# Optimization experiments

Measured on AMD Instinct MI355X. Metric: run time of the kernel, lower is better.

The kernel has to match this reference:

```python
import jax, jax.numpy as jnp
import numpy as np

R0 = 5.0
LEAK = 0.1
N_NODES = 50000
N_EDGES = 1600000
DIM_A = 32
DIM_V = 32


def setup_inputs() -> dict:
    key = jax.random.key(0)
    ks = jax.random.split(key, 10)
    s = 1.0 / np.sqrt(DIM_A)
    return {
        "r_ij": jax.random.normal(ks[0], (N_EDGES, 3), dtype=jnp.float32) * 2.0,
        "res_emb": jax.random.normal(ks[1], (N_NODES, DIM_A), dtype=jnp.float32),
        "src": jax.random.randint(ks[2], (N_EDGES,), 0, N_NODES, dtype=jnp.int64),
        "dst": jax.random.randint(ks[3], (N_EDGES,), 0, N_NODES, dtype=jnp.int64),
        "W1": jax.random.normal(ks[4], (DIM_A, DIM_A), dtype=jnp.float32) * s,
        "b1": jnp.zeros((DIM_A,), dtype=jnp.float32),
        "W2": jax.random.normal(ks[5], (DIM_A, DIM_A), dtype=jnp.float32) * s,
        "b2": jnp.zeros((DIM_A,), dtype=jnp.float32),
        "W3": jax.random.normal(ks[6], (DIM_A, DIM_A), dtype=jnp.float32) * s,
        "Wv": jax.random.normal(ks[7], (DIM_V, DIM_A), dtype=jnp.float32) * s,
    }


def _radial_encode(r, n, rmax):
    # r: [E, 3] -> [E, n]
    hn = (n + 1) // 2
    coeffs = (jnp.pi / rmax) * (1 + jnp.arange(hn) // 2).astype(r.dtype)
    dist = jnp.linalg.norm(r, axis=-1)[..., None]  # [E, 1]
    phase = coeffs * dist                           # [E, hn]
    return jnp.concatenate([jnp.cos(phase), jnp.sin(phase[..., : n - hn])], axis=-1)


def _leaky(x):
    return jnp.where(x >= 0, x, LEAK * x)


def _tens_sigmoid_vec(x):
    # Equivariant saturating nonlinearity on vectors: scale by tanh(|x|)/|x|.
    nrm = jnp.linalg.norm(x, axis=-1, keepdims=True)
    safe = jnp.where(nrm > 0, nrm, 1.0)
    return x * (jnp.tanh(nrm) / safe)


def reference(r_ij, res_emb, src, dst, W1, b1, W2, b2, W3, Wv):
    n_nodes = res_emb.shape[0]
    dim_a = W1.shape[1]
    # gather dst node features onto edges
    res_emb_j = res_emb[dst]                              # [E, dim_a]
    x = _radial_encode(r_ij, dim_a, R0) + res_emb_j       # [E, dim_a]
    h = _leaky(x @ W1.T + b1)
    h = _leaky(h @ W2.T + b2)
    rad_enc_ij = h @ W3.T                                 # [E, dim_a]
    rv = _tens_sigmoid_vec(r_ij * (7.0 / R0))             # [E, 3]
    phi_v = rad_enc_ij[..., None] * rv[:, None, :]        # [E, dim_a, 3]
    A_a = jax.ops.segment_sum(rad_enc_ij, src, num_segments=n_nodes)  # [N, dim_a]
    A_v = jax.ops.segment_sum(phi_v, src, num_segments=n_nodes)       # [N, dim_a, 3]
    out_v = jnp.einsum("nad,va->nvd", A_v, Wv)            # [N, dim_v, 3]
    return A_a, out_v
```

## Files before the change

kernel.cpp:

```cpp
#include <hip/hip_runtime.h>
#include <math.h>


#define NN 50000
#define NE 1600000
#define DA 32
#define PI_R0 0.62831853071795864769f
#define SCAN_BLOCKS 196
#define RSTRIDE 34

typedef float v2f __attribute__((ext_vector_type(2)));
typedef short bf16x8 __attribute__((ext_vector_type(8)));
typedef float f32x16 __attribute__((ext_vector_type(16)));

union frag_u { unsigned u[4]; bf16x8 v; };

__device__ __forceinline__ void wsync() {
    asm volatile("s_waitcnt lgkmcnt(0)" ::: "memory");
}

__device__ __forceinline__ unsigned cvt_pk(float lo, float hi) {
    unsigned r;
    asm("v_cvt_pk_bf16_f32 %0, %1, %2" : "=v"(r) : "v"(lo), "v"(hi));
    return r;
}

__device__ __forceinline__ float leaky(float x) {
    return fmaxf(x, 0.0f) + 0.1f * fminf(x, 0.0f);
}

__device__ __forceinline__ unsigned bf_hi(float x) {
    return (__float_as_uint(x) + 0x8000u) >> 16;
}
__device__ __forceinline__ unsigned bf_pack2(float lo, float hi) {
    return bf_hi(lo) | ((__float_as_uint(hi) + 0x8000u) & 0xffff0000u);
}


__global__ __launch_bounds__(256) void k_hist(const int* __restrict__ src,
                                              int* __restrict__ counts,
                                              int* __restrict__ rank) {
    const int e = blockIdx.x * 256 + threadIdx.x;
    rank[e] = atomicAdd(&counts[src[e]], 1);
}

__global__ __launch_bounds__(256) void k_scanA(const int* __restrict__ counts,
                                               int* __restrict__ bsum) {
    __shared__ int red[256];
    const int t = threadIdx.x;
    const int idx = blockIdx.x * 256 + t;
    red[t] = (idx < NN) ? counts[idx] : 0;
    __syncthreads();
    #pragma unroll
    for (int off = 128; off > 0; off >>= 1) {
        if (t < off) red[t] += red[t + off];
        __syncthreads();
    }
    if (t == 0) bsum[blockIdx.x] = red[0];
}

__global__ __launch_bounds__(256) void k_scanB(const int* __restrict__ bsum,
                                               int* __restrict__ bbase) {
    __shared__ int s[256];
    const int t = threadIdx.x;
    const int v = (t < SCAN_BLOCKS) ? bsum[t] : 0;
    s[t] = v;
    __syncthreads();
    #pragma unroll
    for (int off = 1; off < 256; off <<= 1) {
        const int x = s[t] + ((t >= off) ? s[t - off] : 0);
        __syncthreads();
        s[t] = x;
        __syncthreads();
    }
    if (t < SCAN_BLOCKS) bbase[t] = s[t] - v;
}

__global__ __launch_bounds__(256) void k_scanC(const int* __restrict__ counts,
                                               const int* __restrict__ bbase,
                                               int* __restrict__ offsets) {
    __shared__ int s[256];
    const int t = threadIdx.x;
    const int idx = blockIdx.x * 256 + t;
    const int v = (idx < NN) ? counts[idx] : 0;
    s[t] = v;
    __syncthreads();
    #pragma unroll
    for (int off = 1; off < 256; off <<= 1) {
        const int x = s[t] + ((t >= off) ? s[t - off] : 0);
        __syncthreads();
        s[t] = x;
        __syncthreads();
    }
    const int excl = s[t] - v + bbase[blockIdx.x];
    if (idx < NN) offsets[idx] = excl;
    if (idx == NN - 1) offsets[NN] = excl + v;
}

__global__ __launch_bounds__(256) void k_prep(
    const float* __restrict__ r_ij,
    const int*   __restrict__ src,
    const int*   __restrict__ dst,
    const int*   __restrict__ offsets,
    const int*   __restrict__ rank,
    uint4* __restrict__ rec)
{
    const int e = blockIdx.x * 256 + threadIdx.x;
    const int s = src[e];
    const int slot = offsets[s] + rank[e];

    const float rx = r_ij[(size_t)e*3 + 0];
    const float ry = r_ij[(size_t)e*3 + 1];
    const float rz = r_ij[(size_t)e*3 + 2];
    const float dist = sqrtf(rx*rx + ry*ry + rz*rz);

    const float nq = 1.4f * dist;
    const float e2 = __expf(2.0f * nq);
    const float sc14 = (nq > 0.0f)
        ? 1.4f * (e2 - 1.0f) * __builtin_amdgcn_rcpf((e2 + 1.0f) * nq)
        : 0.0f;

    uint4 r;
    r.x = __float_as_uint(dist);
    r.y = bf_pack2(rx * sc14, ry * sc14);
    r.z = bf_hi(rz * sc14);
    r.w = (unsigned)s | ((unsigned)dst[e] << 16);
    rec[slot] = r;
}

__global__ __launch_bounds__(256) void k_embcvt(const float* __restrict__ emb,
                                                unsigned* __restrict__ emb16) {
    const int t = blockIdx.x * 256 + threadIdx.x;
    emb16[t] = bf_pack2(emb[2*t], emb[2*t + 1]);
}


__global__ __launch_bounds__(256, 2) void dt_window(
    const uint4*    __restrict__ rec,
    const unsigned* __restrict__ emb16,
    const float* __restrict__ W1, const float* __restrict__ b1,
    const float* __restrict__ W2, const float* __restrict__ b2,
    const float* __restrict__ W3,
    float* __restrict__ A_a,
    float* __restrict__ out_v)
{
    __shared__ float  xrad[4][64][RSTRIDE];
    __shared__ float4 rvn_lds[4][64];

    const int tid  = threadIdx.x;
    const int wv   = tid >> 6;
    const int lane = tid & 63;
    const int g    = lane >> 5;
    const int m    = lane & 31;
    const int slot = blockIdx.x * 256 + tid;

    frag_u wf1[2], wf2[2], wf3[2];
    #pragma unroll
    for (int kt = 0; kt < 2; ++kt) {
        const float4 a1 = *(const float4*)&W1[m*DA + 16*kt + 4*g];
        const float4 c1 = *(const float4*)&W1[m*DA + 16*kt + 8 + 4*g];
        wf1[kt].u[0] = cvt_pk(a1.x, a1.y); wf1[kt].u[1] = cvt_pk(a1.z, a1.w);
        wf1[kt].u[2] = cvt_pk(c1.x, c1.y); wf1[kt].u[3] = cvt_pk(c1.z, c1.w);
        const float4 a2 = *(const float4*)&W2[m*DA + 16*kt + 4*g];
        const float4 c2 = *(const float4*)&W2[m*DA + 16*kt + 8 + 4*g];
        wf2[kt].u[0] = cvt_pk(a2.x, a2.y); wf2[kt].u[1] = cvt_pk(a2.z, a2.w);
        wf2[kt].u[2] = cvt_pk(c2.x, c2.y); wf2[kt].u[3] = cvt_pk(c2.z, c2.w);
        const float4 a3 = *(const float4*)&W3[m*DA + 16*kt + 4*g];
        const float4 c3 = *(const float4*)&W3[m*DA + 16*kt + 8 + 4*g];
        wf3[kt].u[0] = cvt_pk(a3.x, a3.y); wf3[kt].u[1] = cvt_pk(a3.z, a3.w);
        wf3[kt].u[2] = cvt_pk(c3.x, c3.y); wf3[kt].u[3] = cvt_pk(c3.z, c3.w);
    }

    const float4 b1q0 = *(const float4*)&b1[4*g];
    const float4 b1q1 = *(const float4*)&b1[8 + 4*g];
    const float4 b1q2 = *(const float4*)&b1[16 + 4*g];
    const float4 b1q3 = *(const float4*)&b1[24 + 4*g];
    const float4 b2q0 = *(const float4*)&b2[4*g];
    const float4 b2q1 = *(const float4*)&b2[8 + 4*g];
    const float4 b2q2 = *(const float4*)&b2[16 + 4*g];
    const float4 b2q3 = *(const float4*)&b2[24 + 4*g];

    const uint4 rc = rec[slot];
    const float dist = __uint_as_float(rc.x);
    const float vx = __uint_as_float(rc.y << 16);
    const float vy = __uint_as_float(rc.y & 0xffff0000u);
    const float vz = __uint_as_float(rc.z << 16);
    const int  node = (int)(rc.w & 0xffffu);
    const int  dn   = (int)(rc.w >> 16);

    v2f xa[16];
    #pragma unroll
    for (int mm = 0; mm < 8; ++mm) {
        float sph, cph;
        __sincosf(PI_R0 * (float)(mm + 1) * dist, &sph, &cph);
        xa[mm]     = (v2f){cph, cph};
        xa[8 + mm] = (v2f){sph, sph};
    }
    const uint4* ep = (const uint4*)(emb16 + (size_t)dn * 16);
    #pragma unroll
    for (int q = 0; q < 4; ++q) {
        const uint4 u = ep[q];
        xa[q*4 + 0] += (v2f){__uint_as_float(u.x << 16), __uint_as_float(u.x & 0xffff0000u)};
        xa[q*4 + 1] += (v2f){__uint_as_float(u.y << 16), __uint_as_float(u.y & 0xffff0000u)};
        xa[q*4 + 2] += (v2f){__uint_as_float(u.z << 16), __uint_as_float(u.z & 0xffff0000u)};
        xa[q*4 + 3] += (v2f){__uint_as_float(u.w << 16), __uint_as_float(u.w & 0xffff0000u)};
    }

    rvn_lds[wv][lane] = make_float4(vx, vy, vz, __int_as_float(node));

    {
        uint2* xr = (uint2*)&xrad[wv][lane][0];
        xr[0] = make_uint2(cvt_pk(xa[0].x,  xa[0].y),  cvt_pk(xa[1].x,  xa[1].y));
        xr[1] = make_uint2(cvt_pk(xa[2].x,  xa[2].y),  cvt_pk(xa[3].x,  xa[3].y));
        xr[2] = make_uint2(cvt_pk(xa[4].x,  xa[4].y),  cvt_pk(xa[5].x,  xa[5].y));
        xr[3] = make_uint2(cvt_pk(xa[6].x,  xa[6].y),  cvt_pk(xa[7].x,  xa[7].y));
        xr[4] = make_uint2(cvt_pk(xa[8].x,  xa[8].y),  cvt_pk(xa[9].x,  xa[9].y));
        xr[5] = make_uint2(cvt_pk(xa[10].x, xa[10].y), cvt_pk(xa[11].x, xa[11].y));
        xr[6] = make_uint2(cvt_pk(xa[12].x, xa[12].y), cvt_pk(xa[13].x, xa[13].y));
        xr[7] = make_uint2(cvt_pk(xa[14].x, xa[14].y), cvt_pk(xa[15].x, xa[15].y));
    }
    wsync();

    frag_u xf[2][2];
    #pragma unroll
    for (int t = 0; t < 2; ++t) {
        const unsigned* er = (const unsigned*)&xrad[wv][32*t + m][0];
        #pragma unroll
        for (int kt = 0; kt < 2; ++kt) {
            const uint2 qa = *(const uint2*)&er[8*kt + 2*g];
            const uint2 qb = *(const uint2*)&er[8*kt + 4 + 2*g];
            xf[t][kt].u[0] = qa.x; xf[t][kt].u[1] = qa.y;
            xf[t][kt].u[2] = qb.x; xf[t][kt].u[3] = qb.y;
        }
    }

    f32x16 acc0, acc1;
    acc0[0]=b1q0.x; acc0[1]=b1q0.y; acc0[2]=b1q0.z; acc0[3]=b1q0.w;
    acc0[4]=b1q1.x; acc0[5]=b1q1.y; acc0[6]=b1q1.z; acc0[7]=b1q1.w;
    acc0[8]=b1q2.x; acc0[9]=b1q2.y; acc0[10]=b1q2.z; acc0[11]=b1q2.w;
    acc0[12]=b1q3.x; acc0[13]=b1q3.y; acc0[14]=b1q3.z; acc0[15]=b1q3.w;
    acc1 = acc0;
    acc0 = __builtin_amdgcn_mfma_f32_32x32x16_bf16(wf1[0].v, xf[0][0].v, acc0, 0, 0, 0);
    acc0 = __builtin_amdgcn_mfma_f32_32x32x16_bf16(wf1[1].v, xf[0][1].v, acc0, 0, 0, 0);
    acc1 = __builtin_amdgcn_mfma_f32_32x32x16_bf16(wf1[0].v, xf[1][0].v, acc1, 0, 0, 0);
    acc1 = __builtin_amdgcn_mfma_f32_32x32x16_bf16(wf1[1].v, xf[1][1].v, acc1, 0, 0, 0);

    frag_u hf[2][2];
    #pragma unroll
    for (int t = 0; t < 2; ++t) {
        const f32x16 a = t ? acc1 : acc0;
        float h[16];
        #pragma unroll
        for (int r = 0; r < 16; ++r) h[r] = leaky(a[r]);
        hf[t][0].u[0] = cvt_pk(h[0], h[1]);   hf[t][0].u[1] = cvt_pk(h[2], h[3]);
        hf[t][0].u[2] = cvt_pk(h[4], h[5]);   hf[t][0].u[3] = cvt_pk(h[6], h[7]);
        hf[t][1].u[0] = cvt_pk(h[8], h[9]);   hf[t][1].u[1] = cvt_pk(h[10], h[11]);
        hf[t][1].u[2] = cvt_pk(h[12], h[13]); hf[t][1].u[3] = cvt_pk(h[14], h[15]);
    }

    f32x16 c0, c1;
    c0[0]=b2q0.x; c0[1]=b2q0.y; c0[2]=b2q0.z; c0[3]=b2q0.w;
    c0[4]=b2q1.x; c0[5]=b2q1.y; c0[6]=b2q1.z; c0[7]=b2q1.w;
    c0[8]=b2q2.x; c0[9]=b2q2.y; c0[10]=b2q2.z; c0[11]=b2q2.w;
    c0[12]=b2q3.x; c0[13]=b2q3.y; c0[14]=b2q3.z; c0[15]=b2q3.w;
    c1 = c0;
    c0 = __builtin_amdgcn_mfma_f32_32x32x16_bf16(wf2[0].v, hf[0][0].v, c0, 0, 0, 0);
    c0 = __builtin_amdgcn_mfma_f32_32x32x16_bf16(wf2[1].v, hf[0][1].v, c0, 0, 0, 0);
    c1 = __builtin_amdgcn_mfma_f32_32x32x16_bf16(wf2[0].v, hf[1][0].v, c1, 0, 0, 0);
    c1 = __builtin_amdgcn_mfma_f32_32x32x16_bf16(wf2[1].v, hf[1][1].v, c1, 0, 0, 0);

    frag_u gf[2][2];
    #pragma unroll
    for (int t = 0; t < 2; ++t) {
        const f32x16 a = t ? c1 : c0;
        float h[16];
        #pragma unroll
        for (int r = 0; r < 16; ++r) h[r] = leaky(a[r]);
        gf[t][0].u[0] = cvt_pk(h[0], h[1]);   gf[t][0].u[1] = cvt_pk(h[2], h[3]);
        gf[t][0].u[2] = cvt_pk(h[4], h[5]);   gf[t][0].u[3] = cvt_pk(h[6], h[7]);
        gf[t][1].u[0] = cvt_pk(h[8], h[9]);   gf[t][1].u[1] = cvt_pk(h[10], h[11]);
        gf[t][1].u[2] = cvt_pk(h[12], h[13]); gf[t][1].u[3] = cvt_pk(h[14], h[15]);
    }

    f32x16 r0 = {}, r1 = {};
    r0 = __builtin_amdgcn_mfma_f32_32x32x16_bf16(wf3[0].v, gf[0][0].v, r0, 0, 0, 0);
    r0 = __builtin_amdgcn_mfma_f32_32x32x16_bf16(wf3[1].v, gf[0][1].v, r0, 0, 0, 0);
    r1 = __builtin_amdgcn_mfma_f32_32x32x16_bf16(wf3[0].v, gf[1][0].v, r1, 0, 0, 0);
    r1 = __builtin_amdgcn_mfma_f32_32x32x16_bf16(wf3[1].v, gf[1][1].v, r1, 0, 0, 0);

    #pragma unroll
    for (int t = 0; t < 2; ++t) {
        const f32x16 a = t ? r1 : r0;
        float* rr = &xrad[wv][32*t + m][0];
        *(float2*)&rr[4*g]          = make_float2(a[0],  a[1]);
        *(float2*)&rr[4*g + 2]      = make_float2(a[2],  a[3]);
        *(float2*)&rr[8 + 4*g]      = make_float2(a[4],  a[5]);
        *(float2*)&rr[8 + 4*g + 2]  = make_float2(a[6],  a[7]);
        *(float2*)&rr[16 + 4*g]     = make_float2(a[8],  a[9]);
        *(float2*)&rr[16 + 4*g + 2] = make_float2(a[10], a[11]);
        *(float2*)&rr[24 + 4*g]     = make_float2(a[12], a[13]);
        *(float2*)&rr[24 + 4*g + 2] = make_float2(a[14], a[15]);
    }
    wsync();

    const int p = lane >> 5;
    const int i = lane & 31;
    const int base = p << 5;

    float accA = 0.0f, a0 = 0.0f, a1 = 0.0f, a2 = 0.0f;
    int cur = __float_as_int(rvn_lds[wv][base].w);

    #pragma unroll 4
    for (int l = 0; l < 32; ++l) {
        const float4 rvn = rvn_lds[wv][base + l];
        const int nd = __float_as_int(rvn.w);
        const float rd = xrad[wv][base + l][i];
        if (nd != cur) {
            atomicAdd(&A_a[cur*DA + i], accA);
            atomicAdd(&out_v[(cur*DA + i)*3 + 0], a0);
            atomicAdd(&out_v[(cur*DA + i)*3 + 1], a1);
            atomicAdd(&out_v[(cur*DA + i)*3 + 2], a2);
            accA = a0 = a1 = a2 = 0.0f;
            cur = nd;
        }
        accA += rd;
        a0 += rd * rvn.x;
        a1 += rd * rvn.y;
        a2 += rd * rvn.z;
    }
    atomicAdd(&A_a[cur*DA + i], accA);
    atomicAdd(&out_v[(cur*DA + i)*3 + 0], a0);
    atomicAdd(&out_v[(cur*DA + i)*3 + 1], a1);
    atomicAdd(&out_v[(cur*DA + i)*3 + 2], a2);
}


__global__ __launch_bounds__(256) void dt_node(
    const float* __restrict__ Wv,
    float* Av_out)
{
    __shared__ float sWv[DA*DA];
    for (int i = threadIdx.x; i < DA*DA; i += 256) sWv[i] = Wv[i];
    __syncthreads();

    const int t = blockIdx.x * 256 + threadIdx.x;
    const int n = t >> 5;
    const int v = t & 31;

    const float* av = Av_out + (size_t)n * (DA*3);
    float o0 = 0.0f, o1 = 0.0f, o2 = 0.0f;
    #pragma unroll
    for (int a = 0; a < DA; ++a) {
        const float w = sWv[v*DA + a];
        o0 += w * av[a*3 + 0];
        o1 += w * av[a*3 + 1];
        o2 += w * av[a*3 + 2];
    }
    __syncthreads();
    float* o = Av_out + (size_t)n * (DA*3) + v*3;
    o[0] = o0; o[1] = o1; o[2] = o2;
}


__global__ __launch_bounds__(256) void k_scan_legacy(const int* __restrict__ counts,
                                                     int* __restrict__ offsets) {
    __shared__ int part[256];
    const int CH = (NN + 255) / 256;
    const int t = threadIdx.x;
    const int base = t * CH;
    int s = 0;
    for (int k = 0; k < CH; ++k) { const int idx = base + k; if (idx < NN) s += counts[idx]; }
    part[t] = s;
    __syncthreads();
    if (t == 0) {
        int run = 0;
        for (int k = 0; k < 256; ++k) { const int v = part[k]; part[k] = run; run += v; }
    }
    __syncthreads();
    int run = part[t];
    for (int k = 0; k < CH; ++k) {
        const int idx = base + k;
        if (idx < NN) { offsets[idx] = run; run += counts[idx]; }
    }
    if (t == 255) offsets[NN] = run;
}

__global__ __launch_bounds__(256) void k_scatter_legacy(const int* __restrict__ src,
                                                        const int* __restrict__ offsets,
                                                        const int* __restrict__ rank,
                                                        int* __restrict__ edge_ids) {
    const int e = blockIdx.x * 256 + threadIdx.x;
    edge_ids[offsets[src[e]] + rank[e]] = e;
}

__global__ __launch_bounds__(256, 2) void dt_window_legacy(
    const float* __restrict__ r_ij,
    const float* __restrict__ res_emb,
    const int*   __restrict__ src,
    const int*   __restrict__ dst,
    const int*   __restrict__ edge_ids,
    const float* __restrict__ W1, const float* __restrict__ b1,
    const float* __restrict__ W2, const float* __restrict__ b2,
    const float* __restrict__ W3,
    float* __restrict__ A_a,
    float* __restrict__ out_v)
{
    __shared__ float  rad_lds[4][32][36];
    __shared__ float4 rvn_lds[4][64];

    const int tid  = threadIdx.x;
    const int wv   = tid >> 6;
    const int lane = tid & 63;
    const int slot = blockIdx.x * 256 + tid;

    const int eid  = edge_ids[slot];
    const int node = src[eid];

    const float rx = r_ij[(size_t)eid*3 + 0];
    const float ry = r_ij[(size_t)eid*3 + 1];
    const float rz = r_ij[(size_t)eid*3 + 2];
    const float dist = sqrtf(rx*rx + ry*ry + rz*rz);

    float xa[DA], xb[DA];
    #pragma unroll
    for (int mm = 0; mm < 8; ++mm) {
        float sph, cph;
        __sincosf(PI_R0 * (float)(mm + 1) * dist, &sph, &cph);
        xa[2*mm] = cph; xa[2*mm+1] = cph;
        xa[16+2*mm] = sph; xa[16+2*mm+1] = sph;
    }
    const float4* er = (const float4*)(res_emb + (size_t)dst[eid] * DA);
    #pragma unroll
    for (int q = 0; q < 8; ++q) {
        const float4 v = er[q];
        xa[q*4+0] += v.x; xa[q*4+1] += v.y; xa[q*4+2] += v.z; xa[q*4+3] += v.w;
    }
    #pragma unroll
    for (int i = 0; i < DA; ++i) {
        float acc = b1[i];
        #pragma unroll
        for (int j = 0; j < DA; ++j) acc += W1[i*DA + j] * xa[j];
        xb[i] = (acc >= 0.0f) ? acc : 0.1f * acc;
    }
    #pragma unroll
    for (int i = 0; i < DA; ++i) {
        float acc = b2[i];
        #pragma unroll
        for (int j = 0; j < DA; ++j) acc += W2[i*DA + j] * xb[j];
        xa[i] = (acc >= 0.0f) ? acc : 0.1f * acc;
    }
    #pragma unroll
    for (int i = 0; i < DA; ++i) {
        float acc = 0.0f;
        #pragma unroll
        for (int j = 0; j < DA; ++j) acc += W3[i*DA + j] * xa[j];
        xb[i] = acc;
    }

    const float qx = rx*1.4f, qy = ry*1.4f, qz = rz*1.4f;
    const float nq = sqrtf(qx*qx + qy*qy + qz*qz);
    const float e2 = __expf(2.0f * nq);
    const float sc = (nq > 0.0f)
        ? (e2 - 1.0f) * __builtin_amdgcn_rcpf((e2 + 1.0f) * nq)
        : 0.0f;

    rvn_lds[wv][lane] = make_float4(qx*sc, qy*sc, qz*sc, __int_as_float(node));

    const int p = lane >> 5;
    const int i = lane & 31;

    if (lane < 32) {
        float* rrow = rad_lds[wv][lane];
        #pragma unroll
        for (int q = 0; q < 8; ++q)
            *(float4*)&rrow[q*4] = make_float4(xb[q*4+0], xb[q*4+1], xb[q*4+2], xb[q*4+3]);
    }
    wsync();

    float accA = 0.0f, a0 = 0.0f, a1 = 0.0f, a2 = 0.0f;
    int cur = __float_as_int(rvn_lds[wv][0].w);

    #pragma unroll 4
    for (int l = 0; l < 32; ++l) {
        const float4 rvn = rvn_lds[wv][l];
        const int nd = __float_as_int(rvn.w);
        const float rd = rad_lds[wv][l][i];
        if (nd != cur) {
            if (p == 0) {
                atomicAdd(&A_a[cur*DA + i], accA);
                atomicAdd(&out_v[(cur*DA + i)*3 + 0], a0);
            } else {
                atomicAdd(&out_v[(cur*DA + i)*3 + 1], a1);
                atomicAdd(&out_v[(cur*DA + i)*3 + 2], a2);
            }
            accA = a0 = a1 = a2 = 0.0f;
            cur = nd;
        }
        accA += rd; a0 += rd*rvn.x; a1 += rd*rvn.y; a2 += rd*rvn.z;
    }
    wsync();
    if (lane >= 32) {
        float* rrow = rad_lds[wv][lane - 32];
        #pragma unroll
        for (int q = 0; q < 8; ++q)
            *(float4*)&rrow[q*4] = make_float4(xb[q*4+0], xb[q*4+1], xb[q*4+2], xb[q*4+3]);
    }
    wsync();
    #pragma unroll 4
    for (int l = 32; l < 64; ++l) {
        const float4 rvn = rvn_lds[wv][l];
        const int nd = __float_as_int(rvn.w);
        const float rd = rad_lds[wv][l - 32][i];
        if (nd != cur) {
            if (p == 0) {
                atomicAdd(&A_a[cur*DA + i], accA);
                atomicAdd(&out_v[(cur*DA + i)*3 + 0], a0);
            } else {
                atomicAdd(&out_v[(cur*DA + i)*3 + 1], a1);
                atomicAdd(&out_v[(cur*DA + i)*3 + 2], a2);
            }
            accA = a0 = a1 = a2 = 0.0f;
            cur = nd;
        }
        accA += rd; a0 += rd*rvn.x; a1 += rd*rvn.y; a2 += rd*rvn.z;
    }
    if (p == 0) {
        atomicAdd(&A_a[cur*DA + i], accA);
        atomicAdd(&out_v[(cur*DA + i)*3 + 0], a0);
    } else {
        atomicAdd(&out_v[(cur*DA + i)*3 + 1], a1);
        atomicAdd(&out_v[(cur*DA + i)*3 + 2], a2);
    }
}


extern "C" void kernel_launch(void* const* d_in, const int* in_sizes, int n_in,
                              void* d_out, int out_size, void* d_ws, size_t ws_size,
                              hipStream_t stream) {
    const float* r_ij    = (const float*)d_in[0];
    const float* res_emb = (const float*)d_in[1];
    const int*   src     = (const int*)d_in[2];
    const int*   dst     = (const int*)d_in[3];
    const float* W1      = (const float*)d_in[4];
    const float* b1      = (const float*)d_in[5];
    const float* W2      = (const float*)d_in[6];
    const float* b2      = (const float*)d_in[7];
    const float* W3      = (const float*)d_in[8];
    const float* Wv      = (const float*)d_in[9];

    float* A_a   = (float*)d_out;
    float* out_v = (float*)d_out + (size_t)NN * DA;

    const size_t need_new = ((size_t)NE*4 + (size_t)NN*16 + NN + NN + 1 + NE + 256 + 256) * sizeof(int);
    const size_t need_leg = ((size_t)NN + NN + 1 + NE + NE) * sizeof(int);

    hipMemsetAsync(d_out, 0, (size_t)out_size * sizeof(float), stream);

    if (ws_size >= need_new) {
        uint4*    rec     = (uint4*)d_ws;
        unsigned* emb16   = (unsigned*)(rec + NE);
        int*      counts  = (int*)(emb16 + (size_t)NN*16);
        int*      offsets = counts + NN;
        int*      rank    = offsets + NN + 1;
        int*      bsum    = rank + NE;
        int*      bbase   = bsum + 256;

        hipMemsetAsync(counts, 0, (size_t)NN * sizeof(int), stream);
        k_hist  <<<NE / 256, 256, 0, stream>>>(src, counts, rank);
        k_scanA <<<SCAN_BLOCKS, 256, 0, stream>>>(counts, bsum);
        k_scanB <<<1, 256, 0, stream>>>(bsum, bbase);
        k_scanC <<<SCAN_BLOCKS, 256, 0, stream>>>(counts, bbase, offsets);
        k_embcvt<<<(NN*16) / 256, 256, 0, stream>>>(res_emb, emb16);
        k_prep  <<<NE / 256, 256, 0, stream>>>(r_ij, src, dst, offsets, rank, rec);
        dt_window<<<NE / 256, 256, 0, stream>>>(rec, emb16,
                                                W1, b1, W2, b2, W3, A_a, out_v);
        dt_node <<<(NN * DA) / 256, 256, 0, stream>>>(Wv, out_v);
    } else if (ws_size >= need_leg) {
        int* counts   = (int*)d_ws;
        int* offsets  = counts + NN;
        int* rank     = offsets + NN + 1;
        int* edge_ids = rank + NE;

        hipMemsetAsync(counts, 0, (size_t)NN * sizeof(int), stream);
        k_hist          <<<NE / 256, 256, 0, stream>>>(src, counts, rank);
        k_scan_legacy   <<<1, 256, 0, stream>>>(counts, offsets);
        k_scatter_legacy<<<NE / 256, 256, 0, stream>>>(src, offsets, rank, edge_ids);
        dt_window_legacy<<<NE / 256, 256, 0, stream>>>(r_ij, res_emb, src, dst, edge_ids,
                                                       W1, b1, W2, b2, W3, A_a, out_v);
        dt_node         <<<(NN * DA) / 256, 256, 0, stream>>>(Wv, out_v);
    }
}
```

Baseline: 260.1 us.

## Split histogram bins per node, process 128 edges per wave, split atomics across half-waves

The counting-sort histogram now uses four sub-bins per source node, keyed by the low bits of the edge index. This spreads atomic contention on the counts array, and the scan is widened to handle the larger bin count. The edge MLP kernel now has each wave process two 64-edge batches and carries the segment accumulator across them, which halves the block count and cuts the flush atomics at batch boundaries. Each half-wave now issues only two of the four output atomics per flush instead of all four. Costs are a longer scan and sub-bins that interleave edges of the same node, though they stay contiguous per node.

```diff
diff --git a/kernel.cpp b/kernel.cpp
--- a/kernel.cpp
+++ b/kernel.cpp
@@ -5,8 +5,9 @@
 #define NN 50000
 #define NE 1600000
 #define DA 32
+#define NB (NN*4)
 #define PI_R0 0.62831853071795864769f
-#define SCAN_BLOCKS 196
+#define SCANB_BLOCKS 782
 #define RSTRIDE 34
 
 typedef float v2f __attribute__((ext_vector_type(2)));
@@ -41,7 +42,8 @@
                                               int* __restrict__ counts,
                                               int* __restrict__ rank) {
     const int e = blockIdx.x * 256 + threadIdx.x;
-    rank[e] = atomicAdd(&counts[src[e]], 1);
+    const int key = (src[e] << 2) | (e & 3);
+    rank[e] = atomicAdd(&counts[key], 1);
 }
 
 __global__ __launch_bounds__(256) void k_scanA(const int* __restrict__ counts,
@@ -49,7 +51,7 @@
     __shared__ int red[256];
     const int t = threadIdx.x;
     const int idx = blockIdx.x * 256 + t;
-    red[t] = (idx < NN) ? counts[idx] : 0;
+    red[t] = (idx < NB) ? counts[idx] : 0;
     __syncthreads();
     #pragma unroll
     for (int off = 128; off > 0; off >>= 1) {
@@ -59,21 +61,21 @@
     if (t == 0) bsum[blockIdx.x] = red[0];
 }
 
-__global__ __launch_bounds__(256) void k_scanB(const int* __restrict__ bsum,
-                                               int* __restrict__ bbase) {
-    __shared__ int s[256];
+__global__ __launch_bounds__(1024) void k_scanB(const int* __restrict__ bsum,
+                                                int* __restrict__ bbase) {
+    __shared__ int s[1024];
     const int t = threadIdx.x;
-    const int v = (t < SCAN_BLOCKS) ? bsum[t] : 0;
+    const int v = (t < SCANB_BLOCKS) ? bsum[t] : 0;
     s[t] = v;
     __syncthreads();
     #pragma unroll
-    for (int off = 1; off < 256; off <<= 1) {
+    for (int off = 1; off < 1024; off <<= 1) {
         const int x = s[t] + ((t >= off) ? s[t - off] : 0);
         __syncthreads();
         s[t] = x;
         __syncthreads();
     }
-    if (t < SCAN_BLOCKS) bbase[t] = s[t] - v;
+    if (t < SCANB_BLOCKS) bbase[t] = s[t] - v;
 }
 
 __global__ __launch_bounds__(256) void k_scanC(const int* __restrict__ counts,
@@ -82,7 +84,7 @@
     __shared__ int s[256];
     const int t = threadIdx.x;
     const int idx = blockIdx.x * 256 + t;
-    const int v = (idx < NN) ? counts[idx] : 0;
+    const int v = (idx < NB) ? counts[idx] : 0;
     s[t] = v;
     __syncthreads();
     #pragma unroll
@@ -93,8 +95,8 @@
         __syncthreads();
     }
     const int excl = s[t] - v + bbase[blockIdx.x];
-    if (idx < NN) offsets[idx] = excl;
-    if (idx == NN - 1) offsets[NN] = excl + v;
+    if (idx < NB) offsets[idx] = excl;
+    if (idx == NB - 1) offsets[NB] = excl + v;
 }
 
 __global__ __launch_bounds__(256) void k_prep(
@@ -107,7 +109,7 @@
 {
     const int e = blockIdx.x * 256 + threadIdx.x;
     const int s = src[e];
-    const int slot = offsets[s] + rank[e];
+    const int slot = offsets[(s << 2) | (e & 3)] + rank[e];
 
     const float rx = r_ij[(size_t)e*3 + 0];
     const float ry = r_ij[(size_t)e*3 + 1];
@@ -147,12 +149,12 @@
     __shared__ float  xrad[4][64][RSTRIDE];
     __shared__ float4 rvn_lds[4][64];
 
-    const int tid  = threadIdx.x;
-    const int wv   = tid >> 6;
-    const int lane = tid & 63;
-    const int g    = lane >> 5;
-    const int m    = lane & 31;
-    const int slot = blockIdx.x * 256 + tid;
+    const int tid   = threadIdx.x;
+    const int wv    = tid >> 6;
+    const int lane  = tid & 63;
+    const int g     = lane >> 5;
+    const int m     = lane & 31;
+    const int wbase = blockIdx.x * 512 + wv * 128;
 
     frag_u wf1[2], wf2[2], wf3[2];
     #pragma unroll
@@ -180,158 +182,171 @@
     const float4 b2q2 = *(const float4*)&b2[16 + 4*g];
     const float4 b2q3 = *(const float4*)&b2[24 + 4*g];
 
-    const uint4 rc = rec[slot];
-    const float dist = __uint_as_float(rc.x);
-    const float vx = __uint_as_float(rc.y << 16);
-    const float vy = __uint_as_float(rc.y & 0xffff0000u);
-    const float vz = __uint_as_float(rc.z << 16);
-    const int  node = (int)(rc.w & 0xffffu);
-    const int  dn   = (int)(rc.w >> 16);
-
-    v2f xa[16];
-    #pragma unroll
-    for (int mm = 0; mm < 8; ++mm) {
-        float sph, cph;
-        __sincosf(PI_R0 * (float)(mm + 1) * dist, &sph, &cph);
-        xa[mm]     = (v2f){cph, cph};
-        xa[8 + mm] = (v2f){sph, sph};
-    }
-    const uint4* ep = (const uint4*)(emb16 + (size_t)dn * 16);
-    #pragma unroll
-    for (int q = 0; q < 4; ++q) {
-        const uint4 u = ep[q];
-        xa[q*4 + 0] += (v2f){__uint_as_float(u.x << 16), __uint_as_float(u.x & 0xffff0000u)};
-        xa[q*4 + 1] += (v2f){__uint_as_float(u.y << 16), __uint_as_float(u.y & 0xffff0000u)};
-        xa[q*4 + 2] += (v2f){__uint_as_float(u.z << 16), __uint_as_float(u.z & 0xffff0000u)};
-        xa[q*4 + 3] += (v2f){__uint_as_float(u.w << 16), __uint_as_float(u.w & 0xffff0000u)};
-    }
-
-    rvn_lds[wv][lane] = make_float4(vx, vy, vz, __int_as_float(node));
-
-    {
-        uint2* xr = (uint2*)&xrad[wv][lane][0];
-        xr[0] = make_uint2(cvt_pk(xa[0].x,  xa[0].y),  cvt_pk(xa[1].x,  xa[1].y));
-        xr[1] = make_uint2(cvt_pk(xa[2].x,  xa[2].y),  cvt_pk(xa[3].x,  xa[3].y));
-        xr[2] = make_uint2(cvt_pk(xa[4].x,  xa[4].y),  cvt_pk(xa[5].x,  xa[5].y));
-        xr[3] = make_uint2(cvt_pk(xa[6].x,  xa[6].y),  cvt_pk(xa[7].x,  xa[7].y));
-        xr[4] = make_uint2(cvt_pk(xa[8].x,  xa[8].y),  cvt_pk(xa[9].x,  xa[9].y));
-        xr[5] = make_uint2(cvt_pk(xa[10].x, xa[10].y), cvt_pk(xa[11].x, xa[11].y));
-        xr[6] = make_uint2(cvt_pk(xa[12].x, xa[12].y), cvt_pk(xa[13].x, xa[13].y));
-        xr[7] = make_uint2(cvt_pk(xa[14].x, xa[14].y), cvt_pk(xa[15].x, xa[15].y));
-    }
-    wsync();
-
-    frag_u xf[2][2];
-    #pragma unroll
-    for (int t = 0; t < 2; ++t) {
-        const unsigned* er = (const unsigned*)&xrad[wv][32*t + m][0];
-        #pragma unroll
-        for (int kt = 0; kt < 2; ++kt) {
-            const uint2 qa = *(const uint2*)&er[8*kt + 2*g];
-            const uint2 qb = *(const uint2*)&er[8*kt + 4 + 2*g];
-            xf[t][kt].u[0] = qa.x; xf[t][kt].u[1] = qa.y;
-            xf[t][kt].u[2] = qb.x; xf[t][kt].u[3] = qb.y;
-        }
-    }
-
-    f32x16 acc0, acc1;
-    acc0[0]=b1q0.x; acc0[1]=b1q0.y; acc0[2]=b1q0.z; acc0[3]=b1q0.w;
-    acc0[4]=b1q1.x; acc0[5]=b1q1.y; acc0[6]=b1q1.z; acc0[7]=b1q1.w;
-    acc0[8]=b1q2.x; acc0[9]=b1q2.y; acc0[10]=b1q2.z; acc0[11]=b1q2.w;
-    acc0[12]=b1q3.x; acc0[13]=b1q3.y; acc0[14]=b1q3.z; acc0[15]=b1q3.w;
-    acc1 = acc0;
-    acc0 = __builtin_amdgcn_mfma_f32_32x32x16_bf16(wf1[0].v, xf[0][0].v, acc0, 0, 0, 0);
-    acc0 = __builtin_amdgcn_mfma_f32_32x32x16_bf16(wf1[1].v, xf[0][1].v, acc0, 0, 0, 0);
-    acc1 = __builtin_amdgcn_mfma_f32_32x32x16_bf16(wf1[0].v, xf[1][0].v, acc1, 0, 0, 0);
-    acc1 = __builtin_amdgcn_mfma_f32_32x32x16_bf16(wf1[1].v, xf[1][1].v, acc1, 0, 0, 0);
-
-    frag_u hf[2][2];
-    #pragma unroll
-    for (int t = 0; t < 2; ++t) {
-        const f32x16 a = t ? acc1 : acc0;
-        float h[16];
-        #pragma unroll
-        for (int r = 0; r < 16; ++r) h[r] = leaky(a[r]);
-        hf[t][0].u[0] = cvt_pk(h[0], h[1]);   hf[t][0].u[1] = cvt_pk(h[2], h[3]);
-        hf[t][0].u[2] = cvt_pk(h[4], h[5]);   hf[t][0].u[3] = cvt_pk(h[6], h[7]);
-        hf[t][1].u[0] = cvt_pk(h[8], h[9]);   hf[t][1].u[1] = cvt_pk(h[10], h[11]);
-        hf[t][1].u[2] = cvt_pk(h[12], h[13]); hf[t][1].u[3] = cvt_pk(h[14], h[15]);
-    }
-
-    f32x16 c0, c1;
-    c0[0]=b2q0.x; c0[1]=b2q0.y; c0[2]=b2q0.z; c0[3]=b2q0.w;
-    c0[4]=b2q1.x; c0[5]=b2q1.y; c0[6]=b2q1.z; c0[7]=b2q1.w;
-    c0[8]=b2q2.x; c0[9]=b2q2.y; c0[10]=b2q2.z; c0[11]=b2q2.w;
-    c0[12]=b2q3.x; c0[13]=b2q3.y; c0[14]=b2q3.z; c0[15]=b2q3.w;
-    c1 = c0;
-    c0 = __builtin_amdgcn_mfma_f32_32x32x16_bf16(wf2[0].v, hf[0][0].v, c0, 0, 0, 0);
-    c0 = __builtin_amdgcn_mfma_f32_32x32x16_bf16(wf2[1].v, hf[0][1].v, c0, 0, 0, 0);
-    c1 = __builtin_amdgcn_mfma_f32_32x32x16_bf16(wf2[0].v, hf[1][0].v, c1, 0, 0, 0);
-    c1 = __builtin_amdgcn_mfma_f32_32x32x16_bf16(wf2[1].v, hf[1][1].v, c1, 0, 0, 0);
-
-    frag_u gf[2][2];
-    #pragma unroll
-    for (int t = 0; t < 2; ++t) {
-        const f32x16 a = t ? c1 : c0;
-        float h[16];
-        #pragma unroll
-        for (int r = 0; r < 16; ++r) h[r] = leaky(a[r]);
-        gf[t][0].u[0] = cvt_pk(h[0], h[1]);   gf[t][0].u[1] = cvt_pk(h[2], h[3]);
-        gf[t][0].u[2] = cvt_pk(h[4], h[5]);   gf[t][0].u[3] = cvt_pk(h[6], h[7]);
-        gf[t][1].u[0] = cvt_pk(h[8], h[9]);   gf[t][1].u[1] = cvt_pk(h[10], h[11]);
-        gf[t][1].u[2] = cvt_pk(h[12], h[13]); gf[t][1].u[3] = cvt_pk(h[14], h[15]);
-    }
-
-    f32x16 r0 = {}, r1 = {};
-    r0 = __builtin_amdgcn_mfma_f32_32x32x16_bf16(wf3[0].v, gf[0][0].v, r0, 0, 0, 0);
-    r0 = __builtin_amdgcn_mfma_f32_32x32x16_bf16(wf3[1].v, gf[0][1].v, r0, 0, 0, 0);
-    r1 = __builtin_amdgcn_mfma_f32_32x32x16_bf16(wf3[0].v, gf[1][0].v, r1, 0, 0, 0);
-    r1 = __builtin_amdgcn_mfma_f32_32x32x16_bf16(wf3[1].v, gf[1][1].v, r1, 0, 0, 0);
-
-    #pragma unroll
-    for (int t = 0; t < 2; ++t) {
-        const f32x16 a = t ? r1 : r0;
-        float* rr = &xrad[wv][32*t + m][0];
-        *(float2*)&rr[4*g]          = make_float2(a[0],  a[1]);
-        *(float2*)&rr[4*g + 2]      = make_float2(a[2],  a[3]);
-        *(float2*)&rr[8 + 4*g]      = make_float2(a[4],  a[5]);
-        *(float2*)&rr[8 + 4*g + 2]  = make_float2(a[6],  a[7]);
-        *(float2*)&rr[16 + 4*g]     = make_float2(a[8],  a[9]);
-        *(float2*)&rr[16 + 4*g + 2] = make_float2(a[10], a[11]);
-        *(float2*)&rr[24 + 4*g]     = make_float2(a[12], a[13]);
-        *(float2*)&rr[24 + 4*g + 2] = make_float2(a[14], a[15]);
-    }
-    wsync();
-
-    const int p = lane >> 5;
-    const int i = lane & 31;
-    const int base = p << 5;
-
+    const int p = g;
+    const int i = m;
     float accA = 0.0f, a0 = 0.0f, a1 = 0.0f, a2 = 0.0f;
-    int cur = __float_as_int(rvn_lds[wv][base].w);
-
-    #pragma unroll 4
-    for (int l = 0; l < 32; ++l) {
-        const float4 rvn = rvn_lds[wv][base + l];
-        const int nd = __float_as_int(rvn.w);
-        const float rd = xrad[wv][base + l][i];
-        if (nd != cur) {
-            atomicAdd(&A_a[cur*DA + i], accA);
-            atomicAdd(&out_v[(cur*DA + i)*3 + 0], a0);
-            atomicAdd(&out_v[(cur*DA + i)*3 + 1], a1);
-            atomicAdd(&out_v[(cur*DA + i)*3 + 2], a2);
-            accA = a0 = a1 = a2 = 0.0f;
-            cur = nd;
-        }
-        accA += rd;
-        a0 += rd * rvn.x;
-        a1 += rd * rvn.y;
-        a2 += rd * rvn.z;
-    }
-    atomicAdd(&A_a[cur*DA + i], accA);
-    atomicAdd(&out_v[(cur*DA + i)*3 + 0], a0);
-    atomicAdd(&out_v[(cur*DA + i)*3 + 1], a1);
-    atomicAdd(&out_v[(cur*DA + i)*3 + 2], a2);
+    int cur = -1;
+
+    #pragma unroll
+    for (int b = 0; b < 2; ++b) {
+        const int slot = wbase + b*64 + lane;
+
+        const uint4 rc = rec[slot];
+        const float dist = __uint_as_float(rc.x);
+        const float vx = __uint_as_float(rc.y << 16);
+        const float vy = __uint_as_float(rc.y & 0xffff0000u);
+        const float vz = __uint_as_float(rc.z << 16);
+        const int  node = (int)(rc.w & 0xffffu);
+        const int  dn   = (int)(rc.w >> 16);
+
+        v2f xa[16];
+        #pragma unroll
+        for (int mm = 0; mm < 8; ++mm) {
+            float sph, cph;
+            __sincosf(PI_R0 * (float)(mm + 1) * dist, &sph, &cph);
+            xa[mm]     = (v2f){cph, cph};
+            xa[8 + mm] = (v2f){sph, sph};
+        }
+        const uint4* ep = (const uint4*)(emb16 + (size_t)dn * 16);
+        #pragma unroll
+        for (int q = 0; q < 4; ++q) {
+            const uint4 u = ep[q];
+            xa[q*4 + 0] += (v2f){__uint_as_float(u.x << 16), __uint_as_float(u.x & 0xffff0000u)};
+            xa[q*4 + 1] += (v2f){__uint_as_float(u.y << 16), __uint_as_float(u.y & 0xffff0000u)};
+            xa[q*4 + 2] += (v2f){__uint_as_float(u.z << 16), __uint_as_float(u.z & 0xffff0000u)};
+            xa[q*4 + 3] += (v2f){__uint_as_float(u.w << 16), __uint_as_float(u.w & 0xffff0000u)};
+        }
+
+        rvn_lds[wv][lane] = make_float4(vx, vy, vz, __int_as_float(node));
+
+        {
+            uint2* xr = (uint2*)&xrad[wv][lane][0];
+            xr[0] = make_uint2(cvt_pk(xa[0].x,  xa[0].y),  cvt_pk(xa[1].x,  xa[1].y));
+            xr[1] = make_uint2(cvt_pk(xa[2].x,  xa[2].y),  cvt_pk(xa[3].x,  xa[3].y));
+            xr[2] = make_uint2(cvt_pk(xa[4].x,  xa[4].y),  cvt_pk(xa[5].x,  xa[5].y));
+            xr[3] = make_uint2(cvt_pk(xa[6].x,  xa[6].y),  cvt_pk(xa[7].x,  xa[7].y));
+            xr[4] = make_uint2(cvt_pk(xa[8].x,  xa[8].y),  cvt_pk(xa[9].x,  xa[9].y));
+            xr[5] = make_uint2(cvt_pk(xa[10].x, xa[10].y), cvt_pk(xa[11].x, xa[11].y));
+            xr[6] = make_uint2(cvt_pk(xa[12].x, xa[12].y), cvt_pk(xa[13].x, xa[13].y));
+            xr[7] = make_uint2(cvt_pk(xa[14].x, xa[14].y), cvt_pk(xa[15].x, xa[15].y));
+        }
+        wsync();
+
+        frag_u xf[2][2];
+        #pragma unroll
+        for (int t = 0; t < 2; ++t) {
+            const unsigned* er = (const unsigned*)&xrad[wv][32*t + m][0];
+            #pragma unroll
+            for (int kt = 0; kt < 2; ++kt) {
+                const uint2 qa = *(const uint2*)&er[8*kt + 2*g];
+                const uint2 qb = *(const uint2*)&er[8*kt + 4 + 2*g];
+                xf[t][kt].u[0] = qa.x; xf[t][kt].u[1] = qa.y;
+                xf[t][kt].u[2] = qb.x; xf[t][kt].u[3] = qb.y;
+            }
+        }
+
+        f32x16 acc0, acc1;
+        acc0[0]=b1q0.x; acc0[1]=b1q0.y; acc0[2]=b1q0.z; acc0[3]=b1q0.w;
+        acc0[4]=b1q1.x; acc0[5]=b1q1.y; acc0[6]=b1q1.z; acc0[7]=b1q1.w;
+        acc0[8]=b1q2.x; acc0[9]=b1q2.y; acc0[10]=b1q2.z; acc0[11]=b1q2.w;
+        acc0[12]=b1q3.x; acc0[13]=b1q3.y; acc0[14]=b1q3.z; acc0[15]=b1q3.w;
+        acc1 = acc0;
+        acc0 = __builtin_amdgcn_mfma_f32_32x32x16_bf16(wf1[0].v, xf[0][0].v, acc0, 0, 0, 0);
+        acc0 = __builtin_amdgcn_mfma_f32_32x32x16_bf16(wf1[1].v, xf[0][1].v, acc0, 0, 0, 0);
+        acc1 = __builtin_amdgcn_mfma_f32_32x32x16_bf16(wf1[0].v, xf[1][0].v, acc1, 0, 0, 0);
+        acc1 = __builtin_amdgcn_mfma_f32_32x32x16_bf16(wf1[1].v, xf[1][1].v, acc1, 0, 0, 0);
+
+        frag_u hf[2][2];
+        #pragma unroll
+        for (int t = 0; t < 2; ++t) {
+            const f32x16 a = t ? acc1 : acc0;
+            float h[16];
+            #pragma unroll
+            for (int r = 0; r < 16; ++r) h[r] = leaky(a[r]);
+            hf[t][0].u[0] = cvt_pk(h[0], h[1]);   hf[t][0].u[1] = cvt_pk(h[2], h[3]);
+            hf[t][0].u[2] = cvt_pk(h[4], h[5]);   hf[t][0].u[3] = cvt_pk(h[6], h[7]);
+            hf[t][1].u[0] = cvt_pk(h[8], h[9]);   hf[t][1].u[1] = cvt_pk(h[10], h[11]);
+            hf[t][1].u[2] = cvt_pk(h[12], h[13]); hf[t][1].u[3] = cvt_pk(h[14], h[15]);
+        }
+
+        f32x16 c0, c1;
+        c0[0]=b2q0.x; c0[1]=b2q0.y; c0[2]=b2q0.z; c0[3]=b2q0.w;
+        c0[4]=b2q1.x; c0[5]=b2q1.y; c0[6]=b2q1.z; c0[7]=b2q1.w;
+        c0[8]=b2q2.x; c0[9]=b2q2.y; c0[10]=b2q2.z; c0[11]=b2q2.w;
+        c0[12]=b2q3.x; c0[13]=b2q3.y; c0[14]=b2q3.z; c0[15]=b2q3.w;
+        c1 = c0;
+        c0 = __builtin_amdgcn_mfma_f32_32x32x16_bf16(wf2[0].v, hf[0][0].v, c0, 0, 0, 0);
+        c0 = __builtin_amdgcn_mfma_f32_32x32x16_bf16(wf2[1].v, hf[0][1].v, c0, 0, 0, 0);
+        c1 = __builtin_amdgcn_mfma_f32_32x32x16_bf16(wf2[0].v, hf[1][0].v, c1, 0, 0, 0);
+        c1 = __builtin_amdgcn_mfma_f32_32x32x16_bf16(wf2[1].v, hf[1][1].v, c1, 0, 0, 0);
+
+        frag_u gf[2][2];
+        #pragma unroll
+        for (int t = 0; t < 2; ++t) {
+            const f32x16 a = t ? c1 : c0;
+            float h[16];
+            #pragma unroll
+            for (int r = 0; r < 16; ++r) h[r] = leaky(a[r]);
+            gf[t][0].u[0] = cvt_pk(h[0], h[1]);   gf[t][0].u[1] = cvt_pk(h[2], h[3]);
+            gf[t][0].u[2] = cvt_pk(h[4], h[5]);   gf[t][0].u[3] = cvt_pk(h[6], h[7]);
+            gf[t][1].u[0] = cvt_pk(h[8], h[9]);   gf[t][1].u[1] = cvt_pk(h[10], h[11]);
+            gf[t][1].u[2] = cvt_pk(h[12], h[13]); gf[t][1].u[3] = cvt_pk(h[14], h[15]);
+        }
+
+        f32x16 r0 = {}, r1 = {};
+        r0 = __builtin_amdgcn_mfma_f32_32x32x16_bf16(wf3[0].v, gf[0][0].v, r0, 0, 0, 0);
+        r0 = __builtin_amdgcn_mfma_f32_32x32x16_bf16(wf3[1].v, gf[0][1].v, r0, 0, 0, 0);
+        r1 = __builtin_amdgcn_mfma_f32_32x32x16_bf16(wf3[0].v, gf[1][0].v, r1, 0, 0, 0);
+        r1 = __builtin_amdgcn_mfma_f32_32x32x16_bf16(wf3[1].v, gf[1][1].v, r1, 0, 0, 0);
+
+        #pragma unroll
+        for (int t = 0; t < 2; ++t) {
+            const f32x16 a = t ? r1 : r0;
+            float* rr = &xrad[wv][32*t + m][0];
+            *(float2*)&rr[4*g]          = make_float2(a[0],  a[1]);
+            *(float2*)&rr[4*g + 2]      = make_float2(a[2],  a[3]);
+            *(float2*)&rr[8 + 4*g]      = make_float2(a[4],  a[5]);
+            *(float2*)&rr[8 + 4*g + 2]  = make_float2(a[6],  a[7]);
+            *(float2*)&rr[16 + 4*g]     = make_float2(a[8],  a[9]);
+            *(float2*)&rr[16 + 4*g + 2] = make_float2(a[10], a[11]);
+            *(float2*)&rr[24 + 4*g]     = make_float2(a[12], a[13]);
+            *(float2*)&rr[24 + 4*g + 2] = make_float2(a[14], a[15]);
+        }
+        wsync();
+
+        #pragma unroll 4
+        for (int l = 0; l < 64; ++l) {
+            const float4 rvn = rvn_lds[wv][l];
+            const int nd = __float_as_int(rvn.w);
+            const float rd = xrad[wv][l][i];
+            if (nd != cur) {
+                if (cur >= 0) {
+                    if (p == 0) {
+                        atomicAdd(&A_a[cur*DA + i], accA);
+                        atomicAdd(&out_v[(cur*DA + i)*3 + 0], a0);
+                    } else {
+                        atomicAdd(&out_v[(cur*DA + i)*3 + 1], a1);
+                        atomicAdd(&out_v[(cur*DA + i)*3 + 2], a2);
+                    }
+                }
+                accA = a0 = a1 = a2 = 0.0f;
+                cur = nd;
+            }
+            accA += rd;
+            a0 += rd * rvn.x;
+            a1 += rd * rvn.y;
+            a2 += rd * rvn.z;
+        }
+        wsync();
+    }
+
+    if (p == 0) {
+        atomicAdd(&A_a[cur*DA + i], accA);
+        atomicAdd(&out_v[(cur*DA + i)*3 + 0], a0);
+    } else {
+        atomicAdd(&out_v[(cur*DA + i)*3 + 1], a1);
+        atomicAdd(&out_v[(cur*DA + i)*3 + 2], a2);
+    }
 }
 
 
@@ -361,6 +376,13 @@
     o[0] = o0; o[1] = o1; o[2] = o2;
 }
 
+
+__global__ __launch_bounds__(256) void k_hist_legacy(const int* __restrict__ src,
+                                                     int* __restrict__ counts,
+                                                     int* __restrict__ rank) {
+    const int e = blockIdx.x * 256 + threadIdx.x;
+    rank[e] = atomicAdd(&counts[src[e]], 1);
+}
 
 __global__ __launch_bounds__(256) void k_scan_legacy(const int* __restrict__ counts,
                                                      int* __restrict__ offsets) {
@@ -551,7 +573,7 @@
     float* A_a   = (float*)d_out;
     float* out_v = (float*)d_out + (size_t)NN * DA;
 
-    const size_t need_new = ((size_t)NE*4 + (size_t)NN*16 + NN + NN + 1 + NE + 256 + 256) * sizeof(int);
+    const size_t need_new = ((size_t)NE*4 + (size_t)NN*16 + NB + NB + 1 + NE + 1024 + 1024) * sizeof(int);
     const size_t need_leg = ((size_t)NN + NN + 1 + NE + NE) * sizeof(int);
 
     hipMemsetAsync(d_out, 0, (size_t)out_size * sizeof(float), stream);
@@ -560,19 +582,19 @@
         uint4*    rec     = (uint4*)d_ws;
         unsigned* emb16   = (unsigned*)(rec + NE);
         int*      counts  = (int*)(emb16 + (size_t)NN*16);
-        int*      offsets = counts + NN;
-        int*      rank    = offsets + NN + 1;
+        int*      offsets = counts + NB;
+        int*      rank    = offsets + NB + 1;
         int*      bsum    = rank + NE;
-        int*      bbase   = bsum + 256;
-
-        hipMemsetAsync(counts, 0, (size_t)NN * sizeof(int), stream);
+        int*      bbase   = bsum + 1024;
+
+        hipMemsetAsync(counts, 0, (size_t)NB * sizeof(int), stream);
         k_hist  <<<NE / 256, 256, 0, stream>>>(src, counts, rank);
-        k_scanA <<<SCAN_BLOCKS, 256, 0, stream>>>(counts, bsum);
-        k_scanB <<<1, 256, 0, stream>>>(bsum, bbase);
-        k_scanC <<<SCAN_BLOCKS, 256, 0, stream>>>(counts, bbase, offsets);
+        k_scanA <<<SCANB_BLOCKS, 256, 0, stream>>>(counts, bsum);
+        k_scanB <<<1, 1024, 0, stream>>>(bsum, bbase);
+        k_scanC <<<SCANB_BLOCKS, 256, 0, stream>>>(counts, bbase, offsets);
         k_embcvt<<<(NN*16) / 256, 256, 0, stream>>>(res_emb, emb16);
         k_prep  <<<NE / 256, 256, 0, stream>>>(r_ij, src, dst, offsets, rank, rec);
-        dt_window<<<NE / 256, 256, 0, stream>>>(rec, emb16,
+        dt_window<<<NE / 512, 256, 0, stream>>>(rec, emb16,
                                                 W1, b1, W2, b2, W3, A_a, out_v);
         dt_node <<<(NN * DA) / 256, 256, 0, stream>>>(Wv, out_v);
     } else if (ws_size >= need_leg) {
@@ -582,7 +604,7 @@
         int* edge_ids = rank + NE;
 
         hipMemsetAsync(counts, 0, (size_t)NN * sizeof(int), stream);
-        k_hist          <<<NE / 256, 256, 0, stream>>>(src, counts, rank);
+        k_hist_legacy   <<<NE / 256, 256, 0, stream>>>(src, counts, rank);
         k_scan_legacy   <<<1, 256, 0, stream>>>(counts, offsets);
         k_scatter_legacy<<<NE / 256, 256, 0, stream>>>(src, offsets, rank, edge_ids);
         dt_window_legacy<<<NE / 256, 256, 0, stream>>>(r_ij, res_emb, src, dst, edge_ids,
```

After: 236.5 us. 1.1x faster.
